# Kernel tuning notes

Hardware: AMD Instinct MI355X
Metric: run time of the kernel (lower is better)

Reference implementation:

```python
import jax, jax.numpy as jnp
from jax import lax
import numpy as np

EPS = 1e-5

def _conv_bn(x, w, g, b, m, v):
    # 3x3 VALID conv (no bias) + inference BatchNorm, no relu
    y = lax.conv_general_dilated(x, w, window_strides=(1, 1), padding='VALID',
                                 dimension_numbers=('NCHW', 'OIHW', 'NCHW'))
    inv = g * lax.rsqrt(v + EPS)                      # [C]
    return y * inv[None, :, None, None] + (b - m * inv)[None, :, None, None]

def _xcorr_depthwise(z, x):
    # z: [B,C,hz,wz] kernel, x: [B,C,hx,wx] search -> [B,C,hx-hz+1,wx-wz+1]
    C = z.shape[1]
    def one(zi, xi):
        return lax.conv_general_dilated(xi[None], zi[:, None], (1, 1), 'VALID',
                                        dimension_numbers=('NCHW', 'OIHW', 'NCHW'),
                                        feature_group_count=C)[0]
    return jax.vmap(one)(z, x)

def setup_inputs() -> dict:
    key = jax.random.key(0)
    B, Cin, H = 32, 256, 256
    ks = jax.random.split(key, 30)
    d = {
        'z': jax.random.normal(ks[0], (B, Cin, 8, 8), jnp.float32),
        'x': jax.random.normal(ks[1], (B, Cin, 32, 32), jnp.float32),
    }
    i = 2
    for p in ['cls_z', 'cls_x', 'reg_z', 'reg_x']:
        d[p + '_w'] = 0.01 * jax.random.normal(ks[i], (H, Cin, 3, 3), jnp.float32); i += 1
        d[p + '_g'] = jnp.ones((H,), jnp.float32)
        d[p + '_b'] = jnp.zeros((H,), jnp.float32)
        d[p + '_m'] = 0.1 * jax.random.normal(ks[i], (H,), jnp.float32); i += 1
        d[p + '_v'] = jax.random.uniform(ks[i], (H,), jnp.float32, 0.5, 1.5); i += 1
    return d

def reference(z, x,
              cls_z_w, cls_z_g, cls_z_b, cls_z_m, cls_z_v,
              cls_x_w, cls_x_g, cls_x_b, cls_x_m, cls_x_v,
              reg_z_w, reg_z_g, reg_z_b, reg_z_m, reg_z_v,
              reg_x_w, reg_x_g, reg_x_b, reg_x_m, reg_x_v):
    cls_z = _conv_bn(z, cls_z_w, cls_z_g, cls_z_b, cls_z_m, cls_z_v)
    cls_x = _conv_bn(x, cls_x_w, cls_x_g, cls_x_b, cls_x_m, cls_x_v)
    cls_out = _xcorr_depthwise(cls_z, cls_x)
    reg_z = _conv_bn(z, reg_z_w, reg_z_g, reg_z_b, reg_z_m, reg_z_v)
    reg_x = _conv_bn(x, reg_x_w, reg_x_g, reg_x_b, reg_x_m, reg_x_v)
    reg_out = _xcorr_depthwise(reg_z, reg_x)
    return (cls_out, reg_out)
```

## Files before the change

kernel.cpp:

```cpp
#include <hip/hip_runtime.h>

#define EPS 1e-5f

typedef __attribute__((ext_vector_type(8))) short bf16x8;
typedef __attribute__((ext_vector_type(4))) float f32x4;
typedef __attribute__((ext_vector_type(4))) unsigned short u16x4;
typedef unsigned short ushort_t;

__device__ __forceinline__ ushort_t f2bf(float f) {
  unsigned u = __float_as_uint(f);
  unsigned r = (u + 0x7fffu + ((u >> 16) & 1u)) >> 16;
  return (ushort_t)r;
}
__device__ __forceinline__ float bf2f(ushort_t h) {
  return __uint_as_float((unsigned)h << 16);
}

#define GLDS16(g, l) __builtin_amdgcn_global_load_lds( \
    (const __attribute__((address_space(1))) void*)(g), \
    (__attribute__((address_space(3))) void*)(l), 16, 0, 0)

__global__ __launch_bounds__(256) void pack_kernel(
    const float* __restrict__ x, const float* __restrict__ z,
    const float* __restrict__ wxa, const float* __restrict__ wxb,
    const float* __restrict__ wza, const float* __restrict__ wzb,
    ushort_t* __restrict__ xh, ushort_t* __restrict__ zh,
    ushort_t* __restrict__ Bxo, ushort_t* __restrict__ Bzo)
{
  __shared__ ushort_t t[64 * 260];
  int id = blockIdx.x;
  int tid = threadIdx.x;
  if (id < 1024) {
    int b = id >> 5, h = id & 31;
    const float* src = x + (size_t)b * 262144 + h * 32;
#pragma unroll
    for (int it = 0; it < 8; ++it) {
      int f = it * 256 + tid;
      int c = f >> 3, wq = f & 7;
      float4 v = *reinterpret_cast<const float4*>(src + c * 1024 + wq * 4);
      t[(4 * wq + 0) * 260 + c] = f2bf(v.x);
      t[(4 * wq + 1) * 260 + c] = f2bf(v.y);
      t[(4 * wq + 2) * 260 + c] = f2bf(v.z);
      t[(4 * wq + 3) * 260 + c] = f2bf(v.w);
    }
    __syncthreads();
    ushort_t* dst = xh + (size_t)(b * 32 + h) * 8192;
#pragma unroll
    for (int it = 0; it < 8; ++it) {
      int Q = it * 256 + tid;
      int w = Q >> 6, c0 = (Q & 63) * 4;
      u16x4 pk = *reinterpret_cast<const u16x4*>(&t[w * 260 + c0]);
      *reinterpret_cast<u16x4*>(&dst[w * 256 + c0]) = pk;
    }
  } else if (id < 1056) {
    int b = id - 1024;
    const float* src = z + (size_t)b * 16384;
#pragma unroll
    for (int it = 0; it < 16; ++it) {
      int f = it * 256 + tid;
      int c = f >> 4, hq = f & 15;
      float4 v = *reinterpret_cast<const float4*>(src + c * 64 + hq * 4);
      t[(4 * hq + 0) * 260 + c] = f2bf(v.x);
      t[(4 * hq + 1) * 260 + c] = f2bf(v.y);
      t[(4 * hq + 2) * 260 + c] = f2bf(v.z);
      t[(4 * hq + 3) * 260 + c] = f2bf(v.w);
    }
    __syncthreads();
    ushort_t* dst = zh + (size_t)b * 16384;
#pragma unroll
    for (int it = 0; it < 16; ++it) {
      int Q = it * 256 + tid;
      int hw = Q >> 6, c0 = (Q & 63) * 4;
      u16x4 pk = *reinterpret_cast<const u16x4*>(&t[hw * 260 + c0]);
      *reinterpret_cast<u16x4*>(&dst[hw * 256 + c0]) = pk;
    }
  } else {
    float* tf = reinterpret_cast<float*>(t);
    int wid = id - 1056;
    int isZ = wid >> 9;
    int n   = wid & 511;
    const float* s0 = isZ ? wza : wxa;
    const float* s1 = isZ ? wzb : wxb;
    const float* src = (n < 256 ? s0 : s1) + (size_t)(n & 255) * 2304;
#pragma unroll
    for (int it = 0; it < 3; ++it) {
      int f = it * 256 + tid;
      if (f < 576) {
        float4 v = *reinterpret_cast<const float4*>(src + f * 4);
        *reinterpret_cast<float4*>(&tf[f * 4]) = v;
      }
    }
    __syncthreads();
    ushort_t* dst = (isZ ? Bzo : Bxo) + (size_t)n * 2304;
#pragma unroll
    for (int it = 0; it < 9; ++it) {
      int k = it * 256 + tid;
      int tap = k >> 8, ci = k & 255;
      dst[k] = f2bf(tf[ci * 9 + tap]);
    }
  }
}

template<int OW, int OWH, int IW, int IMG, typename OutT>
__device__ __forceinline__ void conv_body(
    int mtile, int ntile,
    const ushort_t* __restrict__ Aimg, const ushort_t* __restrict__ Bw,
    const float* __restrict__ g0, const float* __restrict__ b0,
    const float* __restrict__ m0, const float* __restrict__ v0,
    const float* __restrict__ g1, const float* __restrict__ b1,
    const float* __restrict__ m1, const float* __restrict__ v1,
    OutT* __restrict__ out0, OutT* __restrict__ out1,
    ushort_t* lds)
{
  const int tid  = threadIdx.x;
  const int lane = tid & 63;
  const int wave = tid >> 6;
  const int wr   = wave >> 1, wc = wave & 1;

  const int chunk = (tid & 7) ^ ((tid >> 3) & 7);
  int abase[4], bbase[4];
#pragma unroll
  for (int i = 0; i < 4; ++i) {
    int row = i * 32 + (tid >> 3);
    int m_g = mtile * 128 + row;
    int b   = m_g / OWH;
    int s   = m_g - b * OWH;
    int oh  = s / OW;
    int ow  = s - oh * OW;
    abase[i] = (b * IMG + oh * IW + ow) * 256 + chunk * 8;
    int n_g = ntile * 128 + row;
    bbase[i] = n_g * 2304 + chunk * 8;
  }

  auto stage = [&](int buf, int ks) {
    const int k0  = ks * 64;
    const int tap = k0 >> 8;
    const int ci0 = k0 & 255;
    const int kh  = tap / 3;
    const int kw  = tap - kh * 3;
    const int aoff = (kh * IW + kw) * 256 + ci0;
    ushort_t* dstA = lds + buf * 16384;
    ushort_t* dstB = dstA + 8192;
#pragma unroll
    for (int i = 0; i < 4; ++i) {
      GLDS16(Aimg + abase[i] + aoff, &dstA[(i * 256 + tid) * 8]);
      GLDS16(Bw + bbase[i] + k0,     &dstB[(i * 256 + tid) * 8]);
    }
  };

  f32x4 acc[4][4];
#pragma unroll
  for (int i = 0; i < 4; ++i)
#pragma unroll
    for (int j = 0; j < 4; ++j)
      acc[i][j] = (f32x4){0.f, 0.f, 0.f, 0.f};

  const int lrow = lane & 15;
  const int lk   = lane >> 4;
  const int rA   = wr * 64;
  const int rB   = wc * 64;
  const int sw   = lrow & 7;

  stage(0, 0);
  __syncthreads();

  for (int ks = 0; ks < 36; ++ks) {
    const int cur = ks & 1;
    if (ks < 35) stage(cur ^ 1, ks + 1);
    const ushort_t* As = lds + cur * 16384;
    const ushort_t* Bs = As + 8192;
#pragma unroll
    for (int kc = 0; kc < 2; ++kc) {
      bf16x8 af[4], bfr[4];
#pragma unroll
      for (int mi = 0; mi < 4; ++mi)
        af[mi] = *(const bf16x8*)&As[(rA + mi * 16 + lrow) * 64 + (((kc << 2) | lk) ^ sw) * 8];
#pragma unroll
      for (int ni = 0; ni < 4; ++ni)
        bfr[ni] = *(const bf16x8*)&Bs[(rB + ni * 16 + lrow) * 64 + (((kc << 2) | lk) ^ sw) * 8];
#pragma unroll
      for (int mi = 0; mi < 4; ++mi)
#pragma unroll
        for (int ni = 0; ni < 4; ++ni)
          acc[mi][ni] = __builtin_amdgcn_mfma_f32_16x16x32_bf16(
              af[mi], bfr[ni], acc[mi][ni], 0, 0, 0);
    }
    __syncthreads();
  }

#pragma unroll
  for (int ni = 0; ni < 4; ++ni) {
    int n_g  = ntile * 128 + rB + ni * 16 + lrow;
    int path = n_g >> 8;
    int co   = n_g & 255;
    const float* G  = path ? g1 : g0;
    const float* Bb = path ? b1 : b0;
    const float* Mm = path ? m1 : m0;
    const float* Vv = path ? v1 : v0;
    float iv = G[co] * rsqrtf(Vv[co] + EPS);
    float be = Bb[co] - Mm[co] * iv;
    OutT* outp = path ? out1 : out0;
#pragma unroll
    for (int mi = 0; mi < 4; ++mi) {
      int m_g = mtile * 128 + rA + mi * 16 + lk * 4;
      int b   = m_g / OWH;
      int s   = m_g - b * OWH;
      if constexpr (sizeof(OutT) == 2) {
        u16x4 pk;
#pragma unroll
        for (int r = 0; r < 4; ++r) pk[r] = f2bf(acc[mi][ni][r] * iv + be);
        *reinterpret_cast<u16x4*>(&outp[(size_t)(b * 256 + co) * OWH + s]) = pk;
      } else {
        f32x4 pk;
#pragma unroll
        for (int r = 0; r < 4; ++r) pk[r] = acc[mi][ni][r] * iv + be;
        *reinterpret_cast<f32x4*>(&outp[(size_t)(b * 256 + co) * OWH + s]) = pk;
      }
    }
  }
}

__global__ __launch_bounds__(256) void conv_fused_kernel(
    const ushort_t* __restrict__ xh, const ushort_t* __restrict__ zh,
    const ushort_t* __restrict__ Bx, const ushort_t* __restrict__ Bz,
    const float* Gcx, const float* Bcx, const float* Mcx, const float* Vcx,
    const float* Grx, const float* Brx, const float* Mrx, const float* Vrx,
    const float* Gcz, const float* Bcz, const float* Mcz, const float* Vcz,
    const float* Grz, const float* Brz, const float* Mrz, const float* Vrz,
    ushort_t* __restrict__ cls_xf, ushort_t* __restrict__ reg_xf,
    float* __restrict__ cls_zf, float* __restrict__ reg_zf)
{
  __shared__ ushort_t lds[2 * 16384];
  int bid = blockIdx.x;
  if (bid < 900) {
    int xcd = bid & 7, within = bid >> 3;
    int id = (xcd < 4 ? xcd * 113 : 452 + (xcd - 4) * 112) + within;
    conv_body<30, 900, 32, 1024, ushort_t>(id >> 2, id & 3, xh, Bx,
        Gcx, Bcx, Mcx, Vcx, Grx, Brx, Mrx, Vrx, cls_xf, reg_xf, lds);
  } else {
    int j = bid - 900;
    conv_body<6, 36, 8, 64, float>(j >> 2, j & 3, zh, Bz,
        Gcz, Bcz, Mcz, Vcz, Grz, Brz, Mrz, Vrz, cls_zf, reg_zf, lds);
  }
}

__global__ __launch_bounds__(256) void xcorr_kernel(
    const float* __restrict__ cls_zf, const float* __restrict__ reg_zf,
    const ushort_t* __restrict__ cls_xf, const ushort_t* __restrict__ reg_xf,
    float* __restrict__ out)
{
  int bid   = blockIdx.x;
  int path  = bid >> 12;
  int pair0 = (bid & 4095) * 2;
  int tid   = threadIdx.x;
  int half  = tid >> 7;
  int t     = tid & 127;
  int bc    = pair0 + half;
  __shared__ float sx[2][912];
  const float*    zp = (path ? reg_zf : cls_zf) + (size_t)bc * 36;
  const ushort_t* xp = (path ? reg_xf : cls_xf) + (size_t)bc * 900;
  {
    u16x4 v = *reinterpret_cast<const u16x4*>(xp + t * 4);
    sx[half][t * 4 + 0] = bf2f(v[0]);
    sx[half][t * 4 + 1] = bf2f(v[1]);
    sx[half][t * 4 + 2] = bf2f(v[2]);
    sx[half][t * 4 + 3] = bf2f(v[3]);
    if (t < 97) {
      u16x4 w = *reinterpret_cast<const u16x4*>(xp + (t + 128) * 4);
      sx[half][(t + 128) * 4 + 0] = bf2f(w[0]);
      sx[half][(t + 128) * 4 + 1] = bf2f(w[1]);
      sx[half][(t + 128) * 4 + 2] = bf2f(w[2]);
      sx[half][(t + 128) * 4 + 3] = bf2f(w[3]);
    }
  }
  float zreg[36];
#pragma unroll
  for (int i = 0; i < 36; ++i) zreg[i] = zp[i];
  __syncthreads();
  if (t < 125) {
    int p = t / 5, q0 = (t % 5) * 5;
    float a0 = 0.f, a1 = 0.f, a2 = 0.f, a3 = 0.f, a4 = 0.f;
#pragma unroll
    for (int u = 0; u < 6; ++u) {
      const float* row = &sx[half][(p + u) * 30 + q0];
      float xw[10];
#pragma unroll
      for (int w = 0; w < 10; ++w) xw[w] = row[w];
#pragma unroll
      for (int v = 0; v < 6; ++v) {
        float zv = zreg[u * 6 + v];
        a0 += zv * xw[v];
        a1 += zv * xw[v + 1];
        a2 += zv * xw[v + 2];
        a3 += zv * xw[v + 3];
        a4 += zv * xw[v + 4];
      }
    }
    float* op = out + (size_t)path * 5120000 + (size_t)bc * 625 + p * 25 + q0;
    op[0] = a0; op[1] = a1; op[2] = a2; op[3] = a3; op[4] = a4;
  }
}

extern "C" void kernel_launch(void* const* d_in, const int* in_sizes, int n_in,
                              void* d_out, int out_size, void* d_ws, size_t ws_size,
                              hipStream_t stream) {
  const float* z = (const float*)d_in[0];
  const float* x = (const float*)d_in[1];
  const float *W[4], *G[4], *Bb[4], *M[4], *V[4];
  for (int p = 0; p < 4; ++p) {
    W[p]  = (const float*)d_in[2 + p * 5 + 0];
    G[p]  = (const float*)d_in[2 + p * 5 + 1];
    Bb[p] = (const float*)d_in[2 + p * 5 + 2];
    M[p]  = (const float*)d_in[2 + p * 5 + 3];
    V[p]  = (const float*)d_in[2 + p * 5 + 4];
  }

  char* ws = (char*)d_ws;
  ushort_t* xhwc   = (ushort_t*)ws; ws += (size_t)32*32*32*256 * 2;
  ushort_t* zhwc   = (ushort_t*)ws; ws += (size_t)32*8*8*256 * 2;
  ushort_t* Bx     = (ushort_t*)ws; ws += (size_t)512*2304 * 2;
  ushort_t* Bz     = (ushort_t*)ws; ws += (size_t)512*2304 * 2;
  ushort_t* cls_xf = (ushort_t*)ws; ws += (size_t)32*256*900 * 2;
  ushort_t* reg_xf = (ushort_t*)ws; ws += (size_t)32*256*900 * 2;
  float* cls_zf    = (float*)ws;    ws += (size_t)32*256*36 * 4;
  float* reg_zf    = (float*)ws;

  float* outF = (float*)d_out;

  pack_kernel<<<2080, 256, 0, stream>>>(x, z, W[1], W[3], W[0], W[2],
                                        xhwc, zhwc, Bx, Bz);
  conv_fused_kernel<<<936, 256, 0, stream>>>(
      xhwc, zhwc, Bx, Bz,
      G[1], Bb[1], M[1], V[1], G[3], Bb[3], M[3], V[3],
      G[0], Bb[0], M[0], V[0], G[2], Bb[2], M[2], V[2],
      cls_xf, reg_xf, cls_zf, reg_zf);
  xcorr_kernel<<<8192, 256, 0, stream>>>(cls_zf, reg_zf, cls_xf, reg_xf, outF);
}
```

Measured before the change: 240.1 us.

## Enlarge conv tile to 128x256 with 8 waves and triple-buffered LDS pipeline

The fused conv GEMM kernel moves from 128x128 tiles with 4 waves and double buffering to 128x256 tiles with 8 waves, 512 threads and three LDS buffers, prefetching two k-steps ahead. Barriers now use a partial vmcnt wait so loads stay in flight. The larger N tile halves re-reads of the A operand and the deeper pipeline hides global latency. The costs are 144KB of LDS per block (one block per CU) and 468 blocks instead of 936, which lowers occupancy and can worsen tail balance.

```diff
diff --git a/kernel.cpp b/kernel.cpp
--- a/kernel.cpp
+++ b/kernel.cpp
@@ -19,6 +19,19 @@
 #define GLDS16(g, l) __builtin_amdgcn_global_load_lds( \
     (const __attribute__((address_space(1))) void*)(g), \
     (__attribute__((address_space(3))) void*)(l), 16, 0, 0)
+
+__device__ __forceinline__ void wait_bar6() {
+  asm volatile("s_waitcnt vmcnt(6) lgkmcnt(0)" ::: "memory");
+  __builtin_amdgcn_sched_barrier(0);
+  __builtin_amdgcn_s_barrier();
+  __builtin_amdgcn_sched_barrier(0);
+}
+__device__ __forceinline__ void wait_bar0() {
+  asm volatile("s_waitcnt vmcnt(0) lgkmcnt(0)" ::: "memory");
+  __builtin_amdgcn_sched_barrier(0);
+  __builtin_amdgcn_s_barrier();
+  __builtin_amdgcn_sched_barrier(0);
+}
 
 __global__ __launch_bounds__(256) void pack_kernel(
     const float* __restrict__ x, const float* __restrict__ z,
@@ -115,37 +128,42 @@
   const int tid  = threadIdx.x;
   const int lane = tid & 63;
   const int wave = tid >> 6;
-  const int wr   = wave >> 1, wc = wave & 1;
+  const int wr   = wave >> 2, wc = wave & 3;
 
   const int chunk = (tid & 7) ^ ((tid >> 3) & 7);
-  int abase[4], bbase[4];
-#pragma unroll
-  for (int i = 0; i < 4; ++i) {
-    int row = i * 32 + (tid >> 3);
+  int abase[2], bbase[4];
+#pragma unroll
+  for (int i = 0; i < 2; ++i) {
+    int row = i * 64 + (tid >> 3);
     int m_g = mtile * 128 + row;
     int b   = m_g / OWH;
     int s   = m_g - b * OWH;
     int oh  = s / OW;
     int ow  = s - oh * OW;
     abase[i] = (b * IMG + oh * IW + ow) * 256 + chunk * 8;
-    int n_g = ntile * 128 + row;
+  }
+#pragma unroll
+  for (int i = 0; i < 4; ++i) {
+    int row = i * 64 + (tid >> 3);
+    int n_g = ntile * 256 + row;
     bbase[i] = n_g * 2304 + chunk * 8;
   }
 
-  auto stage = [&](int buf, int ks) {
-    const int k0  = ks * 64;
+  auto stage = [&](int buf, int kt) {
+    const int k0  = kt * 64;
     const int tap = k0 >> 8;
     const int ci0 = k0 & 255;
     const int kh  = tap / 3;
     const int kw  = tap - kh * 3;
     const int aoff = (kh * IW + kw) * 256 + ci0;
-    ushort_t* dstA = lds + buf * 16384;
+    ushort_t* dstA = lds + buf * 24576;
     ushort_t* dstB = dstA + 8192;
 #pragma unroll
-    for (int i = 0; i < 4; ++i) {
-      GLDS16(Aimg + abase[i] + aoff, &dstA[(i * 256 + tid) * 8]);
-      GLDS16(Bw + bbase[i] + k0,     &dstB[(i * 256 + tid) * 8]);
-    }
+    for (int i = 0; i < 2; ++i)
+      GLDS16(Aimg + abase[i] + aoff, &dstA[(i * 512 + tid) * 8]);
+#pragma unroll
+    for (int i = 0; i < 4; ++i)
+      GLDS16(Bw + bbase[i] + k0, &dstB[(i * 512 + tid) * 8]);
   };
 
   f32x4 acc[4][4];
@@ -161,13 +179,8 @@
   const int rB   = wc * 64;
   const int sw   = lrow & 7;
 
-  stage(0, 0);
-  __syncthreads();
-
-  for (int ks = 0; ks < 36; ++ks) {
-    const int cur = ks & 1;
-    if (ks < 35) stage(cur ^ 1, ks + 1);
-    const ushort_t* As = lds + cur * 16384;
+  auto compute = [&](int buf) {
+    const ushort_t* As = lds + buf * 24576;
     const ushort_t* Bs = As + 8192;
 #pragma unroll
     for (int kc = 0; kc < 2; ++kc) {
@@ -185,12 +198,28 @@
           acc[mi][ni] = __builtin_amdgcn_mfma_f32_16x16x32_bf16(
               af[mi], bfr[ni], acc[mi][ni], 0, 0, 0);
     }
-    __syncthreads();
-  }
+  };
+
+  stage(0, 0);
+  stage(1, 1);
+  wait_bar6();
+
+  int cb = 0;
+  for (int kt = 0; kt < 34; ++kt) {
+    int sb = (cb == 0) ? 2 : cb - 1;
+    stage(sb, kt + 2);
+    compute(cb);
+    wait_bar6();
+    cb = (cb == 2) ? 0 : cb + 1;
+  }
+  compute(cb);
+  wait_bar0();
+  cb = (cb == 2) ? 0 : cb + 1;
+  compute(cb);
 
 #pragma unroll
   for (int ni = 0; ni < 4; ++ni) {
-    int n_g  = ntile * 128 + rB + ni * 16 + lrow;
+    int n_g  = ntile * 256 + rB + ni * 16 + lrow;
     int path = n_g >> 8;
     int co   = n_g & 255;
     const float* G  = path ? g1 : g0;
@@ -220,7 +249,7 @@
   }
 }
 
-__global__ __launch_bounds__(256) void conv_fused_kernel(
+__global__ __launch_bounds__(512, 1) void conv_fused_kernel(
     const ushort_t* __restrict__ xh, const ushort_t* __restrict__ zh,
     const ushort_t* __restrict__ Bx, const ushort_t* __restrict__ Bz,
     const float* Gcx, const float* Bcx, const float* Mcx, const float* Vcx,
@@ -230,16 +259,16 @@
     ushort_t* __restrict__ cls_xf, ushort_t* __restrict__ reg_xf,
     float* __restrict__ cls_zf, float* __restrict__ reg_zf)
 {
-  __shared__ ushort_t lds[2 * 16384];
-  int bid = blockIdx.x;
-  if (bid < 900) {
-    int xcd = bid & 7, within = bid >> 3;
-    int id = (xcd < 4 ? xcd * 113 : 452 + (xcd - 4) * 112) + within;
-    conv_body<30, 900, 32, 1024, ushort_t>(id >> 2, id & 3, xh, Bx,
+  __shared__ ushort_t lds[3 * 24576];
+  int orig = blockIdx.x;
+  int xcd = orig & 7, local = orig >> 3;
+  int id = (xcd < 4 ? xcd * 59 : 236 + (xcd - 4) * 58) + local;
+  if (id < 450) {
+    conv_body<30, 900, 32, 1024, ushort_t>(id >> 1, id & 1, xh, Bx,
         Gcx, Bcx, Mcx, Vcx, Grx, Brx, Mrx, Vrx, cls_xf, reg_xf, lds);
   } else {
-    int j = bid - 900;
-    conv_body<6, 36, 8, 64, float>(j >> 2, j & 3, zh, Bz,
+    int j = id - 450;
+    conv_body<6, 36, 8, 64, float>(j >> 1, j & 1, zh, Bz,
         Gcz, Bcz, Mcz, Vcz, Grz, Brz, Mrz, Vrz, cls_zf, reg_zf, lds);
   }
 }
@@ -329,7 +358,7 @@
 
   pack_kernel<<<2080, 256, 0, stream>>>(x, z, W[1], W[3], W[0], W[2],
                                         xhwc, zhwc, Bx, Bz);
-  conv_fused_kernel<<<936, 256, 0, stream>>>(
+  conv_fused_kernel<<<468, 512, 0, stream>>>(
       xhwc, zhwc, Bx, Bz,
       G[1], Bb[1], M[1], V[1], G[3], Bb[3], M[3], V[3],
       G[0], Bb[0], M[0], V[0], G[2], Bb[2], M[2], V[2],
```

Result: faster. 228.6 us (-4.8%).
